# Performance work log

Measured on AMD Instinct MI355X. Metric: run time of the kernel, lower is better.

The kernel has to match this reference:

```python
import jax, jax.numpy as jnp
import numpy as np

N_HEADS = 16
N_KV_HEADS = 4
HEAD_DIM = 128
ROPE_BASE = 10000.0


def _rms_norm(x):
    eps = jnp.asarray(jnp.finfo(x.dtype).eps, x.dtype)
    return x * jax.lax.rsqrt(jnp.mean(x * x, axis=-1, keepdims=True) + eps)


def _rope_tables(T, dtype):
    d = HEAD_DIM
    inv_freq = 1.0 / (ROPE_BASE ** (jnp.arange(0, d, 2, dtype=jnp.float32) / d))
    freqs = jnp.outer(jnp.arange(T, dtype=jnp.float32), inv_freq)  # [T, d/2]
    return jnp.cos(freqs).astype(dtype), jnp.sin(freqs).astype(dtype)


def _apply_rope(x, cos, sin):
    # x: [B, H, T, D]; cos/sin: [T, D/2]
    d = x.shape[-1] // 2
    x1, x2 = x[..., :d], x[..., d:]
    return jnp.concatenate((x1 * cos + x2 * sin, -x1 * sin + x2 * cos), axis=-1)


def setup_inputs() -> dict:
    key = jax.random.key(0)
    ks = jax.random.split(key, 5)
    B, T, C = 2, 2048, 2048
    kv_dim = N_KV_HEADS * HEAD_DIM
    s = 0.02
    return {
        "x": jax.random.normal(ks[0], (B, T, C), jnp.float32),
        "Wq": jax.random.normal(ks[1], (C, C), jnp.float32) * s,
        "Wk": jax.random.normal(ks[2], (kv_dim, C), jnp.float32) * s,
        "Wv": jax.random.normal(ks[3], (kv_dim, C), jnp.float32) * s,
        "Wo": jax.random.normal(ks[4], (C, C), jnp.float32) * s,
    }


def reference(x, Wq, Wk, Wv, Wo):
    B, T, C = x.shape
    g = N_HEADS // N_KV_HEADS

    # QKV projections (torch Linear: x @ W.T), split into heads -> [B, H, T, D]
    q = (x @ Wq.T).reshape(B, T, N_HEADS, HEAD_DIM).transpose(0, 2, 1, 3)
    k = (x @ Wk.T).reshape(B, T, N_KV_HEADS, HEAD_DIM).transpose(0, 2, 1, 3)
    v = (x @ Wv.T).reshape(B, T, N_KV_HEADS, HEAD_DIM).transpose(0, 2, 1, 3)

    # QK RMSNorm (no learned weight)
    q, k = _rms_norm(q), _rms_norm(k)

    # RoPE
    cos, sin = _rope_tables(T, q.dtype)
    q, k = _apply_rope(q, cos, sin), _apply_rope(k, cos, sin)

    # GQA: expand kv heads
    k = jnp.repeat(k, g, axis=1)
    v = jnp.repeat(v, g, axis=1)

    # causal SDPA
    scale = 1.0 / jnp.sqrt(jnp.asarray(HEAD_DIM, q.dtype))
    scores = jnp.einsum("bhqd,bhkd->bhqk", q, k) * scale
    mask = jnp.tril(jnp.ones((T, T), bool))
    scores = jnp.where(mask, scores, jnp.asarray(-jnp.inf, scores.dtype))
    att = jax.nn.softmax(scores, axis=-1)
    y = jnp.einsum("bhqk,bhkd->bhqd", att, v)

    y = y.transpose(0, 2, 1, 3).reshape(B, T, C)
    return y @ Wo.T
```

## Files before the change

### kernel.cpp

```cpp
#include <hip/hip_runtime.h>
#include <hip/hip_bf16.h>
#include <cstdint>
#include <math.h>

#define DEVINL __device__ __forceinline__

typedef __attribute__((ext_vector_type(8))) __bf16 bf16x8;
typedef __attribute__((ext_vector_type(4))) float floatx4;

constexpr int TB = 2;
constexpr int TT = 2048;
constexpr int TC = 2048;
constexpr int NH = 16, NKV = 4, HD = 128;
constexpr int MR = TB * TT;
constexpr int NQ = NH * HD;
constexpr int NK = NKV * HD;
constexpr int NQKV = NQ + 2 * NK;

DEVINL unsigned bfbits(float f) {
  unsigned u = __builtin_bit_cast(unsigned, f);
  return (u + 0x7FFFu + ((u >> 16) & 1u)) >> 16;
}
DEVINL int pk2(float a, float b) {
  union { __hip_bfloat162 h; int i; } u;
  u.h = __float22bfloat162_rn(float2{a, b});
  return u.i;
}
DEVINL void gl_lds16(const __hip_bfloat16* g, __hip_bfloat16* l) {
  __builtin_amdgcn_global_load_lds(
      (const __attribute__((address_space(1))) unsigned int*)g,
      (__attribute__((address_space(3))) unsigned int*)l, 16, 0, 0);
}
DEVINL floatx4 mfma16(bf16x8 a, bf16x8 b, floatx4 c) {
  return __builtin_amdgcn_mfma_f32_16x16x32_bf16(a, b, c, 0, 0, 0);
}
DEVINL void cstore(float* p, float v) { *p = v; }
DEVINL void cstore(__hip_bfloat16* p, float v) { *(unsigned short*)p = (unsigned short)bfbits(v); }

__global__ __launch_bounds__(256) void k_cvt5(
    const float* __restrict__ s0, const float* __restrict__ s1,
    const float* __restrict__ s2, const float* __restrict__ s3,
    const float* __restrict__ s4,
    __hip_bfloat16* __restrict__ d0, __hip_bfloat16* __restrict__ d1,
    __hip_bfloat16* __restrict__ d2, __hip_bfloat16* __restrict__ d3,
    __hip_bfloat16* __restrict__ d4) {
  const float* s;
  __hip_bfloat16* d;
  int n;
  switch (blockIdx.y) {
    case 0: s = s0; d = d0; n = MR * TC; break;
    case 1: s = s1; d = d1; n = NQ * TC; break;
    case 2: s = s2; d = d2; n = NK * TC; break;
    case 3: s = s3; d = d3; n = NK * TC; break;
    default: s = s4; d = d4; n = TC * TC; break;
  }
  int i = (blockIdx.x * 256 + threadIdx.x) * 4;
  if (i >= n) return;
  float4 v = *(const float4*)(s + i);
  ushort4 o;
  o.x = (unsigned short)bfbits(v.x);
  o.y = (unsigned short)bfbits(v.y);
  o.z = (unsigned short)bfbits(v.z);
  o.w = (unsigned short)bfbits(v.w);
  *(ushort4*)(d + i) = o;
}

template <typename OUT_T>
__global__ __launch_bounds__(256, 2) void k_gemm_bt(
    const __hip_bfloat16* __restrict__ A, const __hip_bfloat16* __restrict__ B,
    OUT_T* __restrict__ C, int M, int N, int K) {
  __shared__ __align__(16) __hip_bfloat16 As[128 * 64];
  __shared__ __align__(16) __hip_bfloat16 Bs[128 * 64];
  const int tid = threadIdx.x;
  const int lane = tid & 63, w = tid >> 6;
  const int q15 = lane & 15, quad = lane >> 4;
  const int wm = w >> 1, wn = w & 1;
  const int tm = blockIdx.y, tn = blockIdx.x;

  const int r0 = tid >> 3;
  const int csw = ((tid & 7) ^ (r0 & 7)) * 8;
  const __hip_bfloat16* ag = A + (size_t)(tm * 128 + r0) * K + csw;
  const __hip_bfloat16* bg = B + (size_t)(tn * 128 + r0) * K + csw;
  __hip_bfloat16* lA = As + (tid & ~63) * 8;
  __hip_bfloat16* lB = Bs + (tid & ~63) * 8;

  floatx4 acc[4][4] = {};
  for (int k0 = 0; k0 < K; k0 += 64) {
    __syncthreads();
#pragma unroll
    for (int i = 0; i < 4; i++) {
      gl_lds16(ag + (size_t)(i * 32) * K + k0, lA + i * 2048);
      gl_lds16(bg + (size_t)(i * 32) * K + k0, lB + i * 2048);
    }
    __syncthreads();
#pragma unroll
    for (int kh = 0; kh < 2; kh++) {
      bf16x8 af[4], bfr[4];
#pragma unroll
      for (int i = 0; i < 4; i++)
        af[i] = *(const bf16x8*)(As + (wm * 64 + i * 16 + q15) * 64 +
                                 (((kh * 4 + quad) ^ (q15 & 7)) * 8));
#pragma unroll
      for (int i = 0; i < 4; i++)
        bfr[i] = *(const bf16x8*)(Bs + (wn * 64 + i * 16 + q15) * 64 +
                                  (((kh * 4 + quad) ^ (q15 & 7)) * 8));
#pragma unroll
      for (int mi = 0; mi < 4; mi++)
#pragma unroll
        for (int ni = 0; ni < 4; ni++)
          acc[mi][ni] = mfma16(af[mi], bfr[ni], acc[mi][ni]);
    }
  }
#pragma unroll
  for (int mi = 0; mi < 4; mi++) {
    int row0 = tm * 128 + wm * 64 + mi * 16 + quad * 4;
#pragma unroll
    for (int ni = 0; ni < 4; ni++) {
      int col = tn * 128 + wn * 64 + ni * 16 + q15;
#pragma unroll
      for (int r = 0; r < 4; r++)
        cstore(C + (size_t)(row0 + r) * N + col, acc[mi][ni][r]);
    }
  }
}

constexpr int ROPE_BLOCKS = (MR * 20) / 4;
__global__ __launch_bounds__(256) void k_prep(
    const __hip_bfloat16* __restrict__ qkv,
    __hip_bfloat16* __restrict__ q_l, __hip_bfloat16* __restrict__ k_l,
    __hip_bfloat16* __restrict__ vt) {
  if (blockIdx.x < ROPE_BLOCKS) {
    int gw = (blockIdx.x * 256 + threadIdx.x) >> 6;
    int lane = threadIdx.x & 63;
    int head = gw % 20;
    int bt = gw / 20;
    int b = bt >> 11, t = bt & (TT - 1);
    bool isq = head < NH;
    int h = isq ? head : head - NH;
    const __hip_bfloat16* src = qkv + (size_t)bt * NQKV + (isq ? h * HD : NQ + h * HD);
    float x1 = __bfloat162float(src[lane]);
    float x2 = __bfloat162float(src[lane + 64]);
    float ss = x1 * x1 + x2 * x2;
#pragma unroll
    for (int m = 1; m < 64; m <<= 1) ss += __shfl_xor(ss, m, 64);
    float rinv = rsqrtf(ss * (1.0f / 128.0f) + 1.1920928955078125e-07f);
    float ang = (float)t * exp2f((float)lane * -(13.287712379549449f / 64.0f));
    float sv = sinf(ang), cv = cosf(ang);
    float scale = isq ? (1.4426950408889634f * 0.08838834764831845f) : 1.0f;
    float o1 = (x1 * cv + x2 * sv) * rinv * scale;
    float o2 = (x2 * cv - x1 * sv) * rinv * scale;
    __hip_bfloat16* dst = isq ? q_l + ((size_t)(b * NH + h) * TT + t) * HD
                              : k_l + ((size_t)(b * NKV + h) * TT + t) * HD;
    *(unsigned short*)(dst + lane) = (unsigned short)bfbits(o1);
    *(unsigned short*)(dst + lane + 64) = (unsigned short)bfbits(o2);
  } else {
    __shared__ __hip_bfloat16 tile[64][130];
    int bid = blockIdx.x - ROPE_BLOCKS;
    int t0 = (bid & 31) * 64;
    int hk = (bid >> 5) & 3;
    int b = bid >> 7;
    int tid = threadIdx.x;
#pragma unroll
    for (int j = 0; j < 32; j++) {
      int e = j * 256 + tid;
      int tt = e >> 7, d = e & 127;
      tile[tt][d] = qkv[(size_t)(b * TT + t0 + tt) * NQKV + NQ + NK + hk * HD + d];
    }
    __syncthreads();
#pragma unroll
    for (int j = 0; j < 32; j++) {
      int e = j * 256 + tid;
      int d = e >> 6, tt = e & 63;
      vt[(((size_t)(b * NKV + hk)) * HD + d) * TT + t0 + tt] = tile[tt][d];
    }
  }
}

__global__ __launch_bounds__(256, 2) void k_attn(
    const __hip_bfloat16* __restrict__ q_l, const __hip_bfloat16* __restrict__ k_l,
    const __hip_bfloat16* __restrict__ vt_l, __hip_bfloat16* __restrict__ y) {
  __shared__ __align__(16) __hip_bfloat16 Ks[2][64 * 128];
  __shared__ __align__(16) __hip_bfloat16 Vs[2][128 * 64];
  __shared__ __align__(16) __hip_bfloat16 Ps[4][32 * 64];
  const int tid = threadIdx.x, lane = tid & 63, w = tid >> 6;
  const int q15 = lane & 15, quad = lane >> 4;
  const int id = blockIdx.x;
  const int sl = id >> 5;
  const int qt = (sl < 8) ? (15 - sl) : (sl - 8);
  const int h = id & 15, b = (id >> 4) & 1;
  const int hk = h >> 2;
  const int nkb = 2 * qt + 2;

  const __hip_bfloat16* kbase = k_l + (size_t)(b * NKV + hk) * TT * HD;
  const __hip_bfloat16* vbase = vt_l + (size_t)(b * NKV + hk) * HD * TT;
  const __hip_bfloat16* qbase = q_l + ((size_t)(b * NH + h) * TT + qt * 128) * HD;

  auto stage = [&](int kb, int buf) {
#pragma unroll
    for (int i = 0; i < 4; i++) {
      int s = i * 256 + tid;
      int rk = s >> 4, ck = s & 15;
      gl_lds16(kbase + (size_t)(kb * 64 + rk) * HD + (ck ^ (rk & 15)) * 8,
               Ks[buf] + (i * 256 + (tid & ~63)) * 8);
      int rv = s >> 3, cv = s & 7;
      gl_lds16(vbase + (size_t)rv * TT + kb * 64 + (cv ^ (rv & 7)) * 8,
               Vs[buf] + (i * 256 + (tid & ~63)) * 8);
    }
  };

  bf16x8 qf[4][2];
#pragma unroll
  for (int dc = 0; dc < 4; dc++)
#pragma unroll
    for (int qh = 0; qh < 2; qh++)
      qf[dc][qh] = *(const bf16x8*)(qbase + (size_t)(w * 32 + qh * 16 + q15) * HD +
                                    dc * 32 + quad * 8);

  __hip_bfloat16* pw = Ps[w];
  const int pw_h = (quad & 1) * 4;

  floatx4 ot[8][2] = {};
  float lsum[2] = {0.0f, 0.0f};
  int cur = 0;
  const int kb_last_w = 2 * qt + (w >> 1);

  for (int kb = 0; kb < nkb; kb++) {
    __syncthreads();
    if (kb == 0) {
      stage(0, cur);
      __syncthreads();
    }
    if (kb + 1 < nkb) stage(kb + 1, cur ^ 1);

    if (kb <= kb_last_w) {
      floatx4 st[4][2] = {};
#pragma unroll
      for (int kt = 0; kt < 4; kt++) {
        int r = kt * 16 + q15;
#pragma unroll
        for (int dc = 0; dc < 4; dc++) {
          int c = dc * 4 + quad;
          bf16x8 kf = *(const bf16x8*)(Ks[cur] + (r * 16 + (c ^ (r & 15))) * 8);
          st[kt][0] = mfma16(kf, qf[dc][0], st[kt][0]);
          st[kt][1] = mfma16(kf, qf[dc][1], st[kt][1]);
        }
      }
      if (kb >= 2 * qt) {
#pragma unroll
        for (int qh = 0; qh < 2; qh++) {
          int qg = qt * 128 + w * 32 + qh * 16 + q15;
#pragma unroll
          for (int kt = 0; kt < 4; kt++)
#pragma unroll
            for (int r = 0; r < 4; r++)
              if (kb * 64 + kt * 16 + quad * 4 + r > qg) st[kt][qh][r] = -INFINITY;
        }
      }
#pragma unroll
      for (int kt = 0; kt < 4; kt++) {
#pragma unroll
        for (int qh = 0; qh < 2; qh++) {
          float p0 = exp2f(st[kt][qh][0]);
          float p1 = exp2f(st[kt][qh][1]);
          float p2 = exp2f(st[kt][qh][2]);
          float p3 = exp2f(st[kt][qh][3]);
          lsum[qh] += (p0 + p1) + (p2 + p3);
          int2 pv;
          pv.x = pk2(p0, p1);
          pv.y = pk2(p2, p3);
          int row = qh * 16 + q15;
          int c4 = (kt * 2 + (quad >> 1)) ^ (row & 7);
          *(int2*)(pw + row * 64 + c4 * 8 + pw_h) = pv;
        }
      }
#pragma unroll
      for (int kc = 0; kc < 2; kc++) {
        bf16x8 pf[2];
#pragma unroll
        for (int qh = 0; qh < 2; qh++) {
          int row = qh * 16 + q15;
          int c4 = (kc * 4 + quad) ^ (row & 7);
          pf[qh] = *(const bf16x8*)(pw + row * 64 + c4 * 8);
        }
#pragma unroll
        for (int dt = 0; dt < 8; dt++) {
          int r = dt * 16 + q15, c = kc * 4 + quad;
          bf16x8 vf = *(const bf16x8*)(Vs[cur] + (r * 8 + (c ^ (r & 7))) * 8);
          ot[dt][0] = mfma16(vf, pf[0], ot[dt][0]);
          ot[dt][1] = mfma16(vf, pf[1], ot[dt][1]);
        }
      }
    }
    cur ^= 1;
  }
#pragma unroll
  for (int qh = 0; qh < 2; qh++) {
    float ls = lsum[qh];
    ls += __shfl_xor(ls, 16, 64);
    ls += __shfl_xor(ls, 32, 64);
    float linv = 1.0f / ls;
    int t = qt * 128 + w * 32 + qh * 16 + q15;
    __hip_bfloat16* yrow = y + (size_t)(b * TT + t) * TC + h * HD;
#pragma unroll
    for (int dt = 0; dt < 8; dt++) {
      int d = dt * 16 + quad * 4;
      ushort4 o;
      o.x = (unsigned short)bfbits(ot[dt][qh][0] * linv);
      o.y = (unsigned short)bfbits(ot[dt][qh][1] * linv);
      o.z = (unsigned short)bfbits(ot[dt][qh][2] * linv);
      o.w = (unsigned short)bfbits(ot[dt][qh][3] * linv);
      *(ushort4*)(yrow + d) = o;
    }
  }
}

extern "C" void kernel_launch(void* const* d_in, const int* in_sizes, int n_in,
                              void* d_out, int out_size, void* d_ws, size_t ws_size,
                              hipStream_t stream) {
  (void)in_sizes; (void)n_in; (void)out_size; (void)ws_size;
  const float* x  = (const float*)d_in[0];
  const float* Wq = (const float*)d_in[1];
  const float* Wk = (const float*)d_in[2];
  const float* Wv = (const float*)d_in[3];
  const float* Wo = (const float*)d_in[4];
  float* out = (float*)d_out;

  char* ws = (char*)d_ws;
  size_t off = 0;
  auto alloc = [&](size_t bytes) {
    void* p = ws + off;
    off += (bytes + 255) & ~(size_t)255;
    return p;
  };
  __hip_bfloat16* xb   = (__hip_bfloat16*)alloc((size_t)MR * TC * 2);
  __hip_bfloat16* wqkv = (__hip_bfloat16*)alloc((size_t)NQKV * TC * 2);
  __hip_bfloat16* wo   = (__hip_bfloat16*)alloc((size_t)TC * TC * 2);
  __hip_bfloat16* qkv  = (__hip_bfloat16*)alloc((size_t)MR * NQKV * 2);
  __hip_bfloat16* q_l  = (__hip_bfloat16*)alloc((size_t)TB * NH * TT * HD * 2);
  __hip_bfloat16* k_l  = (__hip_bfloat16*)alloc((size_t)TB * NKV * TT * HD * 2);
  __hip_bfloat16* vt_l = (__hip_bfloat16*)alloc((size_t)TB * NKV * HD * TT * 2);
  __hip_bfloat16* yb   = (__hip_bfloat16*)alloc((size_t)MR * TC * 2);

  k_cvt5<<<dim3((MR * TC / 4 + 255) / 256, 5), 256, 0, stream>>>(
      x, Wq, Wk, Wv, Wo,
      xb, wqkv, wqkv + (size_t)NQ * TC, wqkv + (size_t)(NQ + NK) * TC, wo);

  k_gemm_bt<__hip_bfloat16><<<dim3(NQKV / 128, MR / 128), 256, 0, stream>>>(
      xb, wqkv, qkv, MR, NQKV, TC);

  k_prep<<<ROPE_BLOCKS + TB * NKV * (TT / 64), 256, 0, stream>>>(qkv, q_l, k_l, vt_l);

  k_attn<<<(TT / 128) * NH * TB, 256, 0, stream>>>(q_l, k_l, vt_l, yb);

  k_gemm_bt<float><<<dim3(TC / 128, MR / 128), 256, 0, stream>>>(
      yb, wo, out, MR, TC, TC);
}
```

Before: 311.5 us.

## Use 256x256 tiled, 8-wave pipelined GEMM for QKV projection

Adds a new GEMM kernel for the QKV projection with 256x256 output tiles, 512 threads and double-buffered LDS. It issues staged global-to-LDS loads interleaved with four quarter MFMA blocks separated by barriers, and raises wave priority during the MFMA blocks. The larger tiles raise arithmetic intensity and the staged loads are meant to overlap memory traffic with compute. In exchange the grid shrinks to 12x16 blocks, which may leave CUs underused, and the many barriers add synchronisation cost.

```diff
diff --git a/kernel.cpp b/kernel.cpp
--- a/kernel.cpp
+++ b/kernel.cpp
@@ -36,6 +36,11 @@
 }
 DEVINL void cstore(float* p, float v) { *p = v; }
 DEVINL void cstore(__hip_bfloat16* p, float v) { *(unsigned short*)p = (unsigned short)bfbits(v); }
+DEVINL void bar() {
+  asm volatile("" ::: "memory");
+  __builtin_amdgcn_s_barrier();
+  asm volatile("" ::: "memory");
+}
 
 __global__ __launch_bounds__(256) void k_cvt5(
     const float* __restrict__ s0, const float* __restrict__ s1,
@@ -119,6 +124,121 @@
       int col = tn * 128 + wn * 64 + ni * 16 + q15;
 #pragma unroll
       for (int r = 0; r < 4; r++)
+        cstore(C + (size_t)(row0 + r) * N + col, acc[mi][ni][r]);
+    }
+  }
+}
+
+__global__ __launch_bounds__(512, 1) void k_gemm256(
+    const __hip_bfloat16* __restrict__ A, const __hip_bfloat16* __restrict__ B,
+    __hip_bfloat16* __restrict__ C, int M, int N, int K) {
+  __shared__ __align__(16) __hip_bfloat16 As[2][256 * 64];
+  __shared__ __align__(16) __hip_bfloat16 Bs[2][256 * 64];
+  const int tid = threadIdx.x;
+  const int lane = tid & 63, w = tid >> 6;
+  const int q15 = lane & 15, quad = lane >> 4;
+  const int wm = w >> 2, wn = w & 3;
+  const int tm = blockIdx.y, tn = blockIdx.x;
+
+  const int r0 = tid >> 3;
+  const int csw = ((tid & 7) ^ (r0 & 7)) * 8;
+  const __hip_bfloat16* ag = A + (size_t)(tm * 256 + r0) * K + csw;
+  const __hip_bfloat16* bg = B + (size_t)(tn * 256 + r0) * K + csw;
+  const int ldst = (tid & ~63) * 8;
+
+  auto stA = [&](int kt, int buf, int c) {
+    gl_lds16(ag + (size_t)(c * 64) * K + kt * 64, &As[buf][c * 4096 + ldst]);
+  };
+  auto stB = [&](int kt, int buf, int c) {
+    gl_lds16(bg + (size_t)(c * 64) * K + kt * 64, &Bs[buf][c * 4096 + ldst]);
+  };
+
+  floatx4 acc[8][4] = {};
+  bf16x8 af[4][2], bfr[4][2];
+  const int NT = K / 64;
+  const int rsw = q15 & 7;
+
+  auto quad_mfma = [&](int mh, int nh) {
+    __builtin_amdgcn_s_setprio(1);
+#pragma unroll
+    for (int mi = 0; mi < 4; ++mi)
+#pragma unroll
+      for (int ni = 0; ni < 2; ++ni)
+#pragma unroll
+        for (int kh = 0; kh < 2; ++kh)
+          acc[mh * 4 + mi][nh * 2 + ni] =
+              mfma16(af[mi][kh], bfr[nh * 2 + ni][kh], acc[mh * 4 + mi][nh * 2 + ni]);
+    __builtin_amdgcn_s_setprio(0);
+  };
+
+#pragma unroll
+  for (int c = 0; c < 4; ++c) { stA(0, 0, c); stB(0, 0, c); }
+#pragma unroll
+  for (int c = 0; c < 4; ++c) stB(1, 1, c);
+  stA(1, 1, 0);
+  stA(1, 1, 1);
+  asm volatile("s_waitcnt vmcnt(6)" ::: "memory");
+  bar();
+
+  for (int t = 0; t < NT; ++t) {
+    const int cur = t & 1;
+#pragma unroll
+    for (int i = 0; i < 4; ++i)
+#pragma unroll
+      for (int kh = 0; kh < 2; ++kh)
+        af[i][kh] = *(const bf16x8*)&As[cur][(wm * 128 + i * 16 + q15) * 64 +
+                                            ((kh * 4 + quad) ^ rsw) * 8];
+#pragma unroll
+    for (int n = 0; n < 2; ++n)
+#pragma unroll
+      for (int kh = 0; kh < 2; ++kh)
+        bfr[n][kh] = *(const bf16x8*)&Bs[cur][(wn * 64 + n * 16 + q15) * 64 +
+                                             ((kh * 4 + quad) ^ rsw) * 8];
+    if (t + 1 < NT) { stA(t + 1, cur ^ 1, 2); stA(t + 1, cur ^ 1, 3); }
+    bar();
+    quad_mfma(0, 0);
+    bar();
+#pragma unroll
+    for (int n = 2; n < 4; ++n)
+#pragma unroll
+      for (int kh = 0; kh < 2; ++kh)
+        bfr[n][kh] = *(const bf16x8*)&Bs[cur][(wn * 64 + n * 16 + q15) * 64 +
+                                             ((kh * 4 + quad) ^ rsw) * 8];
+    bar();
+    quad_mfma(0, 1);
+    bar();
+#pragma unroll
+    for (int i = 0; i < 4; ++i)
+#pragma unroll
+      for (int kh = 0; kh < 2; ++kh)
+        af[i][kh] = *(const bf16x8*)&As[cur][(wm * 128 + (i + 4) * 16 + q15) * 64 +
+                                            ((kh * 4 + quad) ^ rsw) * 8];
+    if (t + 2 < NT) { stB(t + 2, cur, 0); stB(t + 2, cur, 1); }
+    bar();
+    quad_mfma(1, 0);
+    bar();
+    if (t + 2 < NT) {
+      stB(t + 2, cur, 2);
+      stB(t + 2, cur, 3);
+      stA(t + 2, cur, 0);
+      stA(t + 2, cur, 1);
+      asm volatile("s_waitcnt vmcnt(6)" ::: "memory");
+    } else if (t + 1 < NT) {
+      asm volatile("s_waitcnt vmcnt(0)" ::: "memory");
+    }
+    bar();
+    quad_mfma(1, 1);
+    bar();
+  }
+
+#pragma unroll
+  for (int mi = 0; mi < 8; ++mi) {
+    int row0 = tm * 256 + wm * 128 + mi * 16 + quad * 4;
+#pragma unroll
+    for (int ni = 0; ni < 4; ++ni) {
+      int col = tn * 256 + wn * 64 + ni * 16 + q15;
+#pragma unroll
+      for (int r = 0; r < 4; ++r)
         cstore(C + (size_t)(row0 + r) * N + col, acc[mi][ni][r]);
     }
   }
@@ -345,7 +465,7 @@
       x, Wq, Wk, Wv, Wo,
       xb, wqkv, wqkv + (size_t)NQ * TC, wqkv + (size_t)(NQ + NK) * TC, wo);
 
-  k_gemm_bt<__hip_bfloat16><<<dim3(NQKV / 128, MR / 128), 256, 0, stream>>>(
+  k_gemm256<<<dim3(NQKV / 256, MR / 256), 512, 0, stream>>>(
       xb, wqkv, qkv, MR, NQKV, TC);
 
   k_prep<<<ROPE_BLOCKS + TB * NKV * (TT / 64), 256, 0, stream>>>(qkv, q_l, k_l, vt_l);
```

Result: no change. 312.9 us (+0.4%).

## Halve attention tiles and pass P through permlane swaps instead of LDS

Applied to the files above, without the earlier changes.

The attention kernel moves from 128-query / 64-key tiles to 64-query / 32-key tiles, with one 16-row query slice per wave, doubling the grid and raising launch bounds to 4 blocks per CU. The P matrix is now rearranged into the MFMA B-operand layout in registers with v_permlane32/16_swap instead of a round trip through shared memory, and the per-block LDS footprint shrinks. The aim is higher occupancy, better load balance across causal tiles, and fewer LDS transfers, at the cost of less K/V reuse per block and more barriers per unit of work.

```diff
diff --git a/kernel.cpp b/kernel.cpp
--- a/kernel.cpp
+++ b/kernel.cpp
@@ -7,6 +7,7 @@
 
 typedef __attribute__((ext_vector_type(8))) __bf16 bf16x8;
 typedef __attribute__((ext_vector_type(4))) float floatx4;
+typedef __attribute__((ext_vector_type(4))) int intx4;
 
 constexpr int TB = 2;
 constexpr int TT = 2048;
@@ -176,52 +177,50 @@
   }
 }
 
-__global__ __launch_bounds__(256, 2) void k_attn(
+__global__ __launch_bounds__(256, 4) void k_attn(
     const __hip_bfloat16* __restrict__ q_l, const __hip_bfloat16* __restrict__ k_l,
     const __hip_bfloat16* __restrict__ vt_l, __hip_bfloat16* __restrict__ y) {
-  __shared__ __align__(16) __hip_bfloat16 Ks[2][64 * 128];
-  __shared__ __align__(16) __hip_bfloat16 Vs[2][128 * 64];
-  __shared__ __align__(16) __hip_bfloat16 Ps[4][32 * 64];
+  __shared__ __align__(16) __hip_bfloat16 Ks[2][32 * 128];
+  __shared__ __align__(16) __hip_bfloat16 Vs[2][128 * 32];
   const int tid = threadIdx.x, lane = tid & 63, w = tid >> 6;
   const int q15 = lane & 15, quad = lane >> 4;
   const int id = blockIdx.x;
   const int sl = id >> 5;
-  const int qt = (sl < 8) ? (15 - sl) : (sl - 8);
+  const int qt = (sl < 8) ? (31 - sl)
+               : (sl < 16) ? (sl - 8)
+               : (sl < 24) ? (39 - sl)
+                           : (sl - 16);
   const int h = id & 15, b = (id >> 4) & 1;
   const int hk = h >> 2;
   const int nkb = 2 * qt + 2;
 
   const __hip_bfloat16* kbase = k_l + (size_t)(b * NKV + hk) * TT * HD;
   const __hip_bfloat16* vbase = vt_l + (size_t)(b * NKV + hk) * HD * TT;
-  const __hip_bfloat16* qbase = q_l + ((size_t)(b * NH + h) * TT + qt * 128) * HD;
+  const __hip_bfloat16* qbase = q_l + ((size_t)(b * NH + h) * TT + qt * 64) * HD;
 
   auto stage = [&](int kb, int buf) {
 #pragma unroll
-    for (int i = 0; i < 4; i++) {
+    for (int i = 0; i < 2; i++) {
       int s = i * 256 + tid;
       int rk = s >> 4, ck = s & 15;
-      gl_lds16(kbase + (size_t)(kb * 64 + rk) * HD + (ck ^ (rk & 15)) * 8,
+      gl_lds16(kbase + (size_t)(kb * 32 + rk) * HD + (ck ^ (rk & 15)) * 8,
                Ks[buf] + (i * 256 + (tid & ~63)) * 8);
-      int rv = s >> 3, cv = s & 7;
-      gl_lds16(vbase + (size_t)rv * TT + kb * 64 + (cv ^ (rv & 7)) * 8,
+      int rv = s >> 2, cv = s & 3;
+      gl_lds16(vbase + (size_t)rv * TT + kb * 32 + (cv ^ (rv & 3)) * 8,
                Vs[buf] + (i * 256 + (tid & ~63)) * 8);
     }
   };
 
-  bf16x8 qf[4][2];
+  bf16x8 qf[4];
 #pragma unroll
   for (int dc = 0; dc < 4; dc++)
-#pragma unroll
-    for (int qh = 0; qh < 2; qh++)
-      qf[dc][qh] = *(const bf16x8*)(qbase + (size_t)(w * 32 + qh * 16 + q15) * HD +
-                                    dc * 32 + quad * 8);
-
-  __hip_bfloat16* pw = Ps[w];
-  const int pw_h = (quad & 1) * 4;
-
-  floatx4 ot[8][2] = {};
-  float lsum[2] = {0.0f, 0.0f};
+    qf[dc] = *(const bf16x8*)(qbase + (size_t)(w * 16 + q15) * HD + dc * 32 + quad * 8);
+
+  floatx4 ot[8] = {};
+  float lsum = 0.0f;
   int cur = 0;
+  const int qg = qt * 64 + w * 16 + q15;
+  const int qminw = qt * 64 + w * 16;
   const int kb_last_w = 2 * qt + (w >> 1);
 
   for (int kb = 0; kb < nkb; kb++) {
@@ -233,84 +232,70 @@
     if (kb + 1 < nkb) stage(kb + 1, cur ^ 1);
 
     if (kb <= kb_last_w) {
-      floatx4 st[4][2] = {};
-#pragma unroll
-      for (int kt = 0; kt < 4; kt++) {
+      floatx4 st[2] = {};
+#pragma unroll
+      for (int kt = 0; kt < 2; kt++) {
         int r = kt * 16 + q15;
 #pragma unroll
         for (int dc = 0; dc < 4; dc++) {
           int c = dc * 4 + quad;
           bf16x8 kf = *(const bf16x8*)(Ks[cur] + (r * 16 + (c ^ (r & 15))) * 8);
-          st[kt][0] = mfma16(kf, qf[dc][0], st[kt][0]);
-          st[kt][1] = mfma16(kf, qf[dc][1], st[kt][1]);
+          st[kt] = mfma16(kf, qf[dc], st[kt]);
         }
       }
-      if (kb >= 2 * qt) {
-#pragma unroll
-        for (int qh = 0; qh < 2; qh++) {
-          int qg = qt * 128 + w * 32 + qh * 16 + q15;
-#pragma unroll
-          for (int kt = 0; kt < 4; kt++)
-#pragma unroll
-            for (int r = 0; r < 4; r++)
-              if (kb * 64 + kt * 16 + quad * 4 + r > qg) st[kt][qh][r] = -INFINITY;
-        }
-      }
-#pragma unroll
-      for (int kt = 0; kt < 4; kt++) {
-#pragma unroll
-        for (int qh = 0; qh < 2; qh++) {
-          float p0 = exp2f(st[kt][qh][0]);
-          float p1 = exp2f(st[kt][qh][1]);
-          float p2 = exp2f(st[kt][qh][2]);
-          float p3 = exp2f(st[kt][qh][3]);
-          lsum[qh] += (p0 + p1) + (p2 + p3);
-          int2 pv;
-          pv.x = pk2(p0, p1);
-          pv.y = pk2(p2, p3);
-          int row = qh * 16 + q15;
-          int c4 = (kt * 2 + (quad >> 1)) ^ (row & 7);
-          *(int2*)(pw + row * 64 + c4 * 8 + pw_h) = pv;
-        }
-      }
-#pragma unroll
-      for (int kc = 0; kc < 2; kc++) {
-        bf16x8 pf[2];
-#pragma unroll
-        for (int qh = 0; qh < 2; qh++) {
-          int row = qh * 16 + q15;
-          int c4 = (kc * 4 + quad) ^ (row & 7);
-          pf[qh] = *(const bf16x8*)(pw + row * 64 + c4 * 8);
-        }
-#pragma unroll
-        for (int dt = 0; dt < 8; dt++) {
-          int r = dt * 16 + q15, c = kc * 4 + quad;
-          bf16x8 vf = *(const bf16x8*)(Vs[cur] + (r * 8 + (c ^ (r & 7))) * 8);
-          ot[dt][0] = mfma16(vf, pf[0], ot[dt][0]);
-          ot[dt][1] = mfma16(vf, pf[1], ot[dt][1]);
-        }
+      if (kb * 32 + 31 > qminw) {
+#pragma unroll
+        for (int kt = 0; kt < 2; kt++)
+#pragma unroll
+          for (int r = 0; r < 4; r++)
+            if (kb * 32 + kt * 16 + quad * 4 + r > qg) st[kt][r] = -INFINITY;
+      }
+      int pA[2], pB[2];
+#pragma unroll
+      for (int kt = 0; kt < 2; kt++) {
+        float p0 = exp2f(st[kt][0]);
+        float p1 = exp2f(st[kt][1]);
+        float p2 = exp2f(st[kt][2]);
+        float p3 = exp2f(st[kt][3]);
+        lsum += (p0 + p1) + (p2 + p3);
+        pA[kt] = pk2(p0, p1);
+        pB[kt] = pk2(p2, p3);
+      }
+      bf16x8 pf;
+      {
+        int u0 = pA[0], u1 = pA[1], v0 = pB[0], v1 = pB[1];
+        asm("v_permlane32_swap_b32 %0, %1" : "+v"(u0), "+v"(u1));
+        asm("v_permlane16_swap_b32 %0, %1" : "+v"(u0), "+v"(u1));
+        asm("v_permlane32_swap_b32 %0, %1" : "+v"(v0), "+v"(v1));
+        asm("v_permlane16_swap_b32 %0, %1" : "+v"(v0), "+v"(v1));
+        intx4 wi;
+        wi[0] = u0; wi[1] = v0; wi[2] = u1; wi[3] = v1;
+        pf = __builtin_bit_cast(bf16x8, wi);
+      }
+#pragma unroll
+      for (int dt = 0; dt < 8; dt++) {
+        int r = dt * 16 + q15;
+        bf16x8 vf = *(const bf16x8*)(Vs[cur] + (r * 4 + (quad ^ (r & 3))) * 8);
+        ot[dt] = mfma16(vf, pf, ot[dt]);
       }
     }
     cur ^= 1;
   }
-#pragma unroll
-  for (int qh = 0; qh < 2; qh++) {
-    float ls = lsum[qh];
-    ls += __shfl_xor(ls, 16, 64);
-    ls += __shfl_xor(ls, 32, 64);
-    float linv = 1.0f / ls;
-    int t = qt * 128 + w * 32 + qh * 16 + q15;
-    __hip_bfloat16* yrow = y + (size_t)(b * TT + t) * TC + h * HD;
-#pragma unroll
-    for (int dt = 0; dt < 8; dt++) {
-      int d = dt * 16 + quad * 4;
-      ushort4 o;
-      o.x = (unsigned short)bfbits(ot[dt][qh][0] * linv);
-      o.y = (unsigned short)bfbits(ot[dt][qh][1] * linv);
-      o.z = (unsigned short)bfbits(ot[dt][qh][2] * linv);
-      o.w = (unsigned short)bfbits(ot[dt][qh][3] * linv);
-      *(ushort4*)(yrow + d) = o;
-    }
+  float ls = lsum;
+  ls += __shfl_xor(ls, 16, 64);
+  ls += __shfl_xor(ls, 32, 64);
+  float linv = 1.0f / ls;
+  const int t = qt * 64 + w * 16 + q15;
+  __hip_bfloat16* yrow = y + (size_t)(b * TT + t) * TC + h * HD;
+#pragma unroll
+  for (int dt = 0; dt < 8; dt++) {
+    int d = dt * 16 + quad * 4;
+    ushort4 o;
+    o.x = (unsigned short)bfbits(ot[dt][0] * linv);
+    o.y = (unsigned short)bfbits(ot[dt][1] * linv);
+    o.z = (unsigned short)bfbits(ot[dt][2] * linv);
+    o.w = (unsigned short)bfbits(ot[dt][3] * linv);
+    *(ushort4*)(yrow + d) = o;
   }
 }
 
@@ -350,7 +335,7 @@
 
   k_prep<<<ROPE_BLOCKS + TB * NKV * (TT / 64), 256, 0, stream>>>(qkv, q_l, k_l, vt_l);
 
-  k_attn<<<(TT / 128) * NH * TB, 256, 0, stream>>>(q_l, k_l, vt_l, yb);
+  k_attn<<<(TT / 64) * NH * TB, 256, 0, stream>>>(q_l, k_l, vt_l, yb);
 
   k_gemm_bt<float><<<dim3(TC / 128, MR / 128), 256, 0, stream>>>(
       yb, wo, out, MR, TC, TC);
```

After: 313.5 us. About the same (+0.6%).

## Fuse RMSNorm/RoPE/V-transpose into QKV GEMM epilogue; keep P in registers via permlane

Applied to the files above, without the earlier changes.

Replaces the generic QKV GEMM plus separate prep kernel with a dedicated GEMM whose epilogue stages the 128x128 tile in LDS, then applies RMSNorm and RoPE for Q/K heads or transposes V directly into the attention layouts. This removes the intermediate qkv buffer round trip and one kernel launch. Separately, the attention kernel no longer writes P to LDS and reads it back; it rearranges the packed probabilities across lanes with v_permlane32/16_swap instructions to form the MFMA B operand. The epilogue is executed serially per wave (32 rows per wave) and the V transpose writes are strided, which may lengthen the GEMM tail.

```diff
diff --git a/kernel.cpp b/kernel.cpp
--- a/kernel.cpp
+++ b/kernel.cpp
@@ -7,6 +7,7 @@
 
 typedef __attribute__((ext_vector_type(8))) __bf16 bf16x8;
 typedef __attribute__((ext_vector_type(4))) float floatx4;
+typedef __attribute__((ext_vector_type(4))) int intx4;
 
 constexpr int TB = 2;
 constexpr int TT = 2048;
@@ -124,54 +125,101 @@
   }
 }
 
-constexpr int ROPE_BLOCKS = (MR * 20) / 4;
-__global__ __launch_bounds__(256) void k_prep(
-    const __hip_bfloat16* __restrict__ qkv,
+__global__ __launch_bounds__(256, 2) void k_gemm_qkv(
+    const __hip_bfloat16* __restrict__ A, const __hip_bfloat16* __restrict__ B,
     __hip_bfloat16* __restrict__ q_l, __hip_bfloat16* __restrict__ k_l,
     __hip_bfloat16* __restrict__ vt) {
-  if (blockIdx.x < ROPE_BLOCKS) {
-    int gw = (blockIdx.x * 256 + threadIdx.x) >> 6;
-    int lane = threadIdx.x & 63;
-    int head = gw % 20;
-    int bt = gw / 20;
-    int b = bt >> 11, t = bt & (TT - 1);
-    bool isq = head < NH;
-    int h = isq ? head : head - NH;
-    const __hip_bfloat16* src = qkv + (size_t)bt * NQKV + (isq ? h * HD : NQ + h * HD);
-    float x1 = __bfloat162float(src[lane]);
-    float x2 = __bfloat162float(src[lane + 64]);
-    float ss = x1 * x1 + x2 * x2;
-#pragma unroll
-    for (int m = 1; m < 64; m <<= 1) ss += __shfl_xor(ss, m, 64);
-    float rinv = rsqrtf(ss * (1.0f / 128.0f) + 1.1920928955078125e-07f);
-    float ang = (float)t * exp2f((float)lane * -(13.287712379549449f / 64.0f));
-    float sv = sinf(ang), cv = cosf(ang);
-    float scale = isq ? (1.4426950408889634f * 0.08838834764831845f) : 1.0f;
-    float o1 = (x1 * cv + x2 * sv) * rinv * scale;
-    float o2 = (x2 * cv - x1 * sv) * rinv * scale;
-    __hip_bfloat16* dst = isq ? q_l + ((size_t)(b * NH + h) * TT + t) * HD
-                              : k_l + ((size_t)(b * NKV + h) * TT + t) * HD;
-    *(unsigned short*)(dst + lane) = (unsigned short)bfbits(o1);
-    *(unsigned short*)(dst + lane + 64) = (unsigned short)bfbits(o2);
+  constexpr int K = TC;
+  __shared__ __align__(16) __hip_bfloat16 smem[128 * 130];
+  __hip_bfloat16* As = smem;
+  __hip_bfloat16* Bs = smem + 128 * 64;
+  const int tid = threadIdx.x;
+  const int lane = tid & 63, w = tid >> 6;
+  const int q15 = lane & 15, quad = lane >> 4;
+  const int wm = w >> 1, wn = w & 1;
+  const int tm = blockIdx.y, tn = blockIdx.x;
+
+  const int r0 = tid >> 3;
+  const int csw = ((tid & 7) ^ (r0 & 7)) * 8;
+  const __hip_bfloat16* ag = A + (size_t)(tm * 128 + r0) * K + csw;
+  const __hip_bfloat16* bg = B + (size_t)(tn * 128 + r0) * K + csw;
+  __hip_bfloat16* lA = As + (tid & ~63) * 8;
+  __hip_bfloat16* lB = Bs + (tid & ~63) * 8;
+
+  floatx4 acc[4][4] = {};
+  for (int k0 = 0; k0 < K; k0 += 64) {
+    __syncthreads();
+#pragma unroll
+    for (int i = 0; i < 4; i++) {
+      gl_lds16(ag + (size_t)(i * 32) * K + k0, lA + i * 2048);
+      gl_lds16(bg + (size_t)(i * 32) * K + k0, lB + i * 2048);
+    }
+    __syncthreads();
+#pragma unroll
+    for (int kh = 0; kh < 2; kh++) {
+      bf16x8 af[4], bfr[4];
+#pragma unroll
+      for (int i = 0; i < 4; i++)
+        af[i] = *(const bf16x8*)(As + (wm * 64 + i * 16 + q15) * 64 +
+                                 (((kh * 4 + quad) ^ (q15 & 7)) * 8));
+#pragma unroll
+      for (int i = 0; i < 4; i++)
+        bfr[i] = *(const bf16x8*)(Bs + (wn * 64 + i * 16 + q15) * 64 +
+                                  (((kh * 4 + quad) ^ (q15 & 7)) * 8));
+#pragma unroll
+      for (int mi = 0; mi < 4; mi++)
+#pragma unroll
+        for (int ni = 0; ni < 4; ni++)
+          acc[mi][ni] = mfma16(af[mi], bfr[ni], acc[mi][ni]);
+    }
+  }
+
+  __syncthreads();
+#pragma unroll
+  for (int mi = 0; mi < 4; mi++)
+#pragma unroll
+    for (int ni = 0; ni < 4; ni++) {
+      int row = wm * 64 + mi * 16 + quad * 4;
+      int col = wn * 64 + ni * 16 + q15;
+#pragma unroll
+      for (int r = 0; r < 4; r++)
+        *(unsigned short*)(smem + (row + r) * 130 + col) =
+            (unsigned short)bfbits(acc[mi][ni][r]);
+    }
+  __syncthreads();
+
+  const int b = tm >> 4;
+  if (tn < NH + NKV) {
+    const bool isq = tn < NH;
+    const int h = isq ? tn : tn - NH;
+    const float scale = isq ? (1.4426950408889634f * 0.08838834764831845f) : 1.0f;
+    __hip_bfloat16* base = isq ? q_l + (size_t)(b * NH + h) * TT * HD
+                               : k_l + (size_t)(b * NKV + h) * TT * HD;
+    const float ifreq = exp2f((float)lane * -(13.287712379549449f / 64.0f));
+    for (int j = 0; j < 32; ++j) {
+      int row = w * 32 + j;
+      int t = (tm & 15) * 128 + row;
+      float x1 = __bfloat162float(smem[row * 130 + lane]);
+      float x2 = __bfloat162float(smem[row * 130 + 64 + lane]);
+      float ss = x1 * x1 + x2 * x2;
+#pragma unroll
+      for (int m = 1; m < 64; m <<= 1) ss += __shfl_xor(ss, m, 64);
+      float rinv = rsqrtf(ss * (1.0f / 128.0f) + 1.1920928955078125e-07f);
+      float ang = (float)t * ifreq;
+      float sv = sinf(ang), cv = cosf(ang);
+      float o1 = (x1 * cv + x2 * sv) * rinv * scale;
+      float o2 = (x2 * cv - x1 * sv) * rinv * scale;
+      __hip_bfloat16* dst = base + (size_t)t * HD;
+      *(unsigned short*)(dst + lane) = (unsigned short)bfbits(o1);
+      *(unsigned short*)(dst + lane + 64) = (unsigned short)bfbits(o2);
+    }
   } else {
-    __shared__ __hip_bfloat16 tile[64][130];
-    int bid = blockIdx.x - ROPE_BLOCKS;
-    int t0 = (bid & 31) * 64;
-    int hk = (bid >> 5) & 3;
-    int b = bid >> 7;
-    int tid = threadIdx.x;
-#pragma unroll
-    for (int j = 0; j < 32; j++) {
+    const int hv = tn - NH - NKV;
+    __hip_bfloat16* vbase = vt + (size_t)(b * NKV + hv) * HD * TT + (tm & 15) * 128;
+    for (int j = 0; j < 64; ++j) {
       int e = j * 256 + tid;
-      int tt = e >> 7, d = e & 127;
-      tile[tt][d] = qkv[(size_t)(b * TT + t0 + tt) * NQKV + NQ + NK + hk * HD + d];
-    }
-    __syncthreads();
-#pragma unroll
-    for (int j = 0; j < 32; j++) {
-      int e = j * 256 + tid;
-      int d = e >> 6, tt = e & 63;
-      vt[(((size_t)(b * NKV + hk)) * HD + d) * TT + t0 + tt] = tile[tt][d];
+      int d = e >> 7, tt = e & 127;
+      vbase[(size_t)d * TT + tt] = smem[tt * 130 + d];
     }
   }
 }
@@ -181,7 +229,6 @@
     const __hip_bfloat16* __restrict__ vt_l, __hip_bfloat16* __restrict__ y) {
   __shared__ __align__(16) __hip_bfloat16 Ks[2][64 * 128];
   __shared__ __align__(16) __hip_bfloat16 Vs[2][128 * 64];
-  __shared__ __align__(16) __hip_bfloat16 Ps[4][32 * 64];
   const int tid = threadIdx.x, lane = tid & 63, w = tid >> 6;
   const int q15 = lane & 15, quad = lane >> 4;
   const int id = blockIdx.x;
@@ -216,9 +263,6 @@
       qf[dc][qh] = *(const bf16x8*)(qbase + (size_t)(w * 32 + qh * 16 + q15) * HD +
                                     dc * 32 + quad * 8);
 
-  __hip_bfloat16* pw = Ps[w];
-  const int pw_h = (quad & 1) * 4;
-
   floatx4 ot[8][2] = {};
   float lsum[2] = {0.0f, 0.0f};
   int cur = 0;
@@ -256,6 +300,7 @@
               if (kb * 64 + kt * 16 + quad * 4 + r > qg) st[kt][qh][r] = -INFINITY;
         }
       }
+      int pA[2][4], pB[2][4];
 #pragma unroll
       for (int kt = 0; kt < 4; kt++) {
 #pragma unroll
@@ -265,12 +310,8 @@
           float p2 = exp2f(st[kt][qh][2]);
           float p3 = exp2f(st[kt][qh][3]);
           lsum[qh] += (p0 + p1) + (p2 + p3);
-          int2 pv;
-          pv.x = pk2(p0, p1);
-          pv.y = pk2(p2, p3);
-          int row = qh * 16 + q15;
-          int c4 = (kt * 2 + (quad >> 1)) ^ (row & 7);
-          *(int2*)(pw + row * 64 + c4 * 8 + pw_h) = pv;
+          pA[qh][kt] = pk2(p0, p1);
+          pB[qh][kt] = pk2(p2, p3);
         }
       }
 #pragma unroll
@@ -278,9 +319,15 @@
         bf16x8 pf[2];
 #pragma unroll
         for (int qh = 0; qh < 2; qh++) {
-          int row = qh * 16 + q15;
-          int c4 = (kc * 4 + quad) ^ (row & 7);
-          pf[qh] = *(const bf16x8*)(pw + row * 64 + c4 * 8);
+          int u0 = pA[qh][2 * kc], u1 = pA[qh][2 * kc + 1];
+          int v0 = pB[qh][2 * kc], v1 = pB[qh][2 * kc + 1];
+          asm("v_permlane32_swap_b32 %0, %1" : "+v"(u0), "+v"(u1));
+          asm("v_permlane16_swap_b32 %0, %1" : "+v"(u0), "+v"(u1));
+          asm("v_permlane32_swap_b32 %0, %1" : "+v"(v0), "+v"(v1));
+          asm("v_permlane16_swap_b32 %0, %1" : "+v"(v0), "+v"(v1));
+          intx4 wi;
+          wi[0] = u0; wi[1] = v0; wi[2] = u1; wi[3] = v1;
+          pf[qh] = __builtin_bit_cast(bf16x8, wi);
         }
 #pragma unroll
         for (int dt = 0; dt < 8; dt++) {
@@ -335,7 +382,6 @@
   __hip_bfloat16* xb   = (__hip_bfloat16*)alloc((size_t)MR * TC * 2);
   __hip_bfloat16* wqkv = (__hip_bfloat16*)alloc((size_t)NQKV * TC * 2);
   __hip_bfloat16* wo   = (__hip_bfloat16*)alloc((size_t)TC * TC * 2);
-  __hip_bfloat16* qkv  = (__hip_bfloat16*)alloc((size_t)MR * NQKV * 2);
   __hip_bfloat16* q_l  = (__hip_bfloat16*)alloc((size_t)TB * NH * TT * HD * 2);
   __hip_bfloat16* k_l  = (__hip_bfloat16*)alloc((size_t)TB * NKV * TT * HD * 2);
   __hip_bfloat16* vt_l = (__hip_bfloat16*)alloc((size_t)TB * NKV * HD * TT * 2);
@@ -345,10 +391,8 @@
       x, Wq, Wk, Wv, Wo,
       xb, wqkv, wqkv + (size_t)NQ * TC, wqkv + (size_t)(NQ + NK) * TC, wo);
 
-  k_gemm_bt<__hip_bfloat16><<<dim3(NQKV / 128, MR / 128), 256, 0, stream>>>(
-      xb, wqkv, qkv, MR, NQKV, TC);
-
-  k_prep<<<ROPE_BLOCKS + TB * NKV * (TT / 64), 256, 0, stream>>>(qkv, q_l, k_l, vt_l);
+  k_gemm_qkv<<<dim3(NQKV / 128, MR / 128), 256, 0, stream>>>(
+      xb, wqkv, q_l, k_l, vt_l);
 
   k_attn<<<(TT / 128) * NH * TB, 256, 0, stream>>>(q_l, k_l, vt_l, yb);
 
```

After: 290.6 us. 1.07x faster.
